# Performance work log

Hardware: AMD Instinct MI355X
Metric: run time of the kernel (lower is better)

The kernel has to match this reference:

```python
import jax, jax.numpy as jnp
import numpy as np

SIZE = 14          # feature-map side (448 image / stride 32)
IMG_STRIDE = 32    # feature->image coordinate stride
RATIOS = [(4, 4), (3, 5), (5, 3), (6, 6), (5, 7), (7, 5), (8, 8), (6, 10), (10, 6)]
GROUPS = [(0, 3), (3, 6), (6, 9)]   # ratio index ranges per scale group
N_LIST = [3, 2, 1]                   # proposals kept per group (sum = proposalN = 6)
IOU_THRESHS = [0.25, 0.25, 0.25]
WIN_NUMS = [(SIZE - h + 1) * (SIZE - w + 1) for h, w in RATIOS]  # 121,120,120,81,80,80,49,45,45
OFFS = np.cumsum([0] + WIN_NUMS)


def _make_coords():
    # image-space [x0,y0,x1,y1] per window, same order as flattened avgpool outputs
    coords = []
    for h, w in RATIOS:
        Ho, Wo = SIZE - h + 1, SIZE - w + 1
        for i in range(Ho):
            for j in range(Wo):
                x0 = i * IMG_STRIDE - 1
                y0 = j * IMG_STRIDE - 1
                x1 = x0 + h * IMG_STRIDE
                y1 = y0 + w * IMG_STRIDE
                coords.append([max(x0, 0), max(y0, 0), x1, y1])
    return np.asarray(coords, np.int32)  # [741, 4]


def setup_inputs() -> dict:
    key = jax.random.key(0)
    B = 65536
    x = jax.random.normal(key, (B, 1, SIZE, SIZE), dtype=jnp.float32)
    coords = jnp.asarray(_make_coords())
    return {"x": x, "coords": coords, "proposalN": 6}


def _avgpool_scores(x):
    # x: [B,1,H,W] -> concat of flattened VALID avgpools, [B, sum(WIN_NUMS)]
    B = x.shape[0]
    outs = []
    for h, w in RATIOS:
        s = jax.lax.reduce_window(x, 0.0, jax.lax.add, (1, 1, h, w), (1, 1, 1, 1), 'VALID')
        outs.append((s / (h * w)).reshape(B, -1))
    return jnp.concatenate(outs, axis=1)


def _nms_group(scores, coords_f, areas, N, thresh):
    # greedy NMS: repeatedly take argmax of remaining scores, suppress IoU>thresh.
    # Matches the torch/numpy loop (sorted-walk == repeated argmax for distinct scores).
    W = scores.shape[0]
    def step(carry, _):
        mask, last = carry
        any_v = jnp.any(mask)
        idx = jnp.argmax(jnp.where(mask, scores, -jnp.inf)).astype(jnp.int32)
        idx = jnp.where(any_v, idx, last)  # if exhausted, repeat last pick (as original)
        c = coords_f[idx]
        lx = jnp.minimum(coords_f[:, 2], c[2]) - jnp.maximum(coords_f[:, 0], c[0]) + 1.0
        ly = jnp.minimum(coords_f[:, 3], c[3]) - jnp.maximum(coords_f[:, 1], c[1]) + 1.0
        inter = jnp.where((lx < 0) | (ly < 0), 0.0, lx * ly)
        iou = inter / (areas + areas[idx] - inter)
        return (mask & (iou <= thresh), idx), idx
    init = (jnp.ones((W,), dtype=bool), jnp.int32(0))
    _, idxs = jax.lax.scan(step, init, None, length=N)
    return idxs  # [N] int32


def reference(x, coords, proposalN):
    all_scores = _avgpool_scores(x)                 # [B, 741]
    coords_f = coords.astype(jnp.float32)
    areas = (coords_f[:, 2] - coords_f[:, 0] + 1.0) * (coords_f[:, 3] - coords_f[:, 1] + 1.0)
    idx_parts = []
    for g, (a, b) in enumerate(GROUPS):
        s, e = int(OFFS[a]), int(OFFS[b])
        cf, ar = coords_f[s:e], areas[s:e]
        N, t = N_LIST[g], IOU_THRESHS[g]
        f = lambda sc, cf=cf, ar=ar, N=N, t=t: _nms_group(sc, cf, ar, N, t)
        idx_parts.append(jax.vmap(f)(all_scores[:, s:e]) + s)  # [B, N]
    proposalN_indices = jnp.concatenate(idx_parts, axis=1)      # [B, proposalN]
    proposalN_windows_scores = jnp.take_along_axis(all_scores, proposalN_indices, axis=1)
    window_scores = all_scores
    return proposalN_indices, proposalN_windows_scores, window_scores
```

## Files before the change

kernel.cpp:

```cpp
#include <hip/hip_runtime.h>
#include <stdint.h>

#define NW 741
#define NEG_INF_KEY 0x007FFFFFu

typedef float f2 __attribute__((ext_vector_type(2)));

static __device__ __forceinline__ unsigned score_key(float f) {
  const unsigned u = __float_as_uint(f);
  return (u & 0x80000000u) ? ~u : (u | 0x80000000u);
}
static __device__ __forceinline__ float key_score(unsigned k) {
  return __uint_as_float((k & 0x80000000u) ? (k ^ 0x80000000u) : ~k);
}

template<int CTRL>
static __device__ __forceinline__ unsigned max_step(unsigned m) {
  const unsigned t = (unsigned)__builtin_amdgcn_update_dpp(0, (int)m, CTRL, 0xF, 0xF, true);
  return m > t ? m : t;
}
template<int CTRL>
static __device__ __forceinline__ int min_step(int c) {
  const int t = __builtin_amdgcn_update_dpp(0x7fffffff, c, CTRL, 0xF, 0xF, false);
  return c < t ? c : t;
}
static __device__ __forceinline__ void wave_argmax(unsigned& k, int& i) {
  unsigned m = k;
  m = max_step<0x111>(m);
  m = max_step<0x112>(m);
  m = max_step<0x114>(m);
  m = max_step<0x118>(m);
  m = max_step<0x142>(m);
  m = max_step<0x143>(m);
  const unsigned smax = (unsigned)__builtin_amdgcn_readlane((int)m, 63);
  int ci = (k == smax) ? i : 0x7fffffff;
  ci = min_step<0x111>(ci);
  ci = min_step<0x112>(ci);
  ci = min_step<0x114>(ci);
  ci = min_step<0x118>(ci);
  ci = min_step<0x142>(ci);
  ci = min_step<0x143>(ci);
  k = smax;
  i = __builtin_amdgcn_readlane(ci, 63);
}

template<int H, int W, int OFF, int S0>
static __device__ __forceinline__ void slot2(const f2* __restrict__ im2,
                                             float* __restrict__ wrowA,
                                             float* __restrict__ wrowB,
                                             const int lane, const bool hasB,
                                             unsigned& ka, unsigned& kb) {
  constexpr int Wo = 14 - W + 1;
  constexpr int NWIN = (14 - H + 1) * Wo;
  const int o = S0 + lane;
  ka = 0u; kb = 0u;
  if (o < NWIN) {
    const int i = o / Wo, j = o - i * Wo;
    const f2* p = im2 + (i * 14 + j);
    f2 acc = {0.0f, 0.0f};
#pragma unroll
    for (int di = 0; di < H; ++di)
#pragma unroll
      for (int dj = 0; dj < W; ++dj)
        acc += p[di * 14 + dj];
    const float scA = acc.x / (float)(H * W);
    const float scB = acc.y / (float)(H * W);
    wrowA[OFF + o] = scA;
    if (hasB) wrowB[OFF + o] = scB;
    ka = score_key(scA);
    kb = score_key(scB);
  }
}

#define SUP2(KA, KB, SB) {                                          \
    const float4 cb = c_box[(SB) + lane];                           \
    const float ar = (cb.z - cb.x + 1.0f) * (cb.w - cb.y + 1.0f);   \
    float lx = fminf(cb.z, bA.z) - fmaxf(cb.x, bA.x) + 1.0f;        \
    float ly = fminf(cb.w, bA.w) - fmaxf(cb.y, bA.y) + 1.0f;        \
    float in = (lx < 0.0f || ly < 0.0f) ? 0.0f : lx * ly;           \
    if (4.0f * in > ar + aA - in) KA = 0u;                          \
    lx = fminf(cb.z, bB.z) - fmaxf(cb.x, bB.x) + 1.0f;              \
    ly = fminf(cb.w, bB.w) - fmaxf(cb.y, bB.y) + 1.0f;              \
    in = (lx < 0.0f || ly < 0.0f) ? 0.0f : lx * ly;                 \
    if (4.0f * in > ar + aB - in) KB = 0u; }

#define SCAN6(bk, bi, K0, K1, K2, K3, K4, K5, S0, S1, S2, S3, S4, S5) \
    bk = K0; bi = (S0) + lane;                                        \
    if (K1 > bk) { bk = K1; bi = (S1) + lane; }                       \
    if (K2 > bk) { bk = K2; bi = (S2) + lane; }                       \
    if (K3 > bk) { bk = K3; bi = (S3) + lane; }                       \
    if (K4 > bk) { bk = K4; bi = (S4) + lane; }                       \
    if (K5 > bk) { bk = K5; bi = (S5) + lane; }

#define SELPICK(bk, bi, last, lastS, idx, sc)                 \
    if (bk > NEG_INF_KEY) { idx = bi; sc = key_score(bk); }   \
    else { idx = last; sc = lastS; }                          \
    last = idx; lastS = sc;

__global__ __launch_bounds__(256) void appm_kernel(
    const float* __restrict__ x, const int* __restrict__ coords,
    float* __restrict__ out, int B) {

  __shared__ float4 c_box[NW];
  __shared__ f2 imgp[4][196];

  const int t = threadIdx.x;
  const int wv = t >> 6;
  const int lane = t & 63;
  const int img0 = blockIdx.x * 8;
  const int imgA = img0 + wv * 2;
  const int imgB = imgA + 1;
  const bool hasA = (imgA < B);
  const bool hasB = (imgB < B);

  for (int w = t; w < NW; w += 256) {
    const int4 c = ((const int4*)coords)[w];
    c_box[w] = make_float4((float)c.x, (float)c.y, (float)c.z, (float)c.w);
  }

  {
    int nimg = B - img0; if (nimg > 8) nimg = 8;
    const float* xb = x + (long long)img0 * 196;
    for (int u = t; u < 784; u += 256) {
      const int pr = u / 196, k = u - pr * 196;
      const int iA = 2 * pr, iB = iA + 1;
      f2 v;
      v.x = (iA < nimg) ? xb[iA * 196 + k] : 0.0f;
      v.y = (iB < nimg) ? xb[iB * 196 + k] : 0.0f;
      imgp[pr][k] = v;
    }
  }
  __syncthreads();

  if (hasA) {
    const f2* im2 = imgp[wv];
    float* wrowA = out + (long long)B * 12 + (long long)imgA * NW;
    float* wrowB = wrowA + NW;

    float myIA = 0.0f, mySA = 0.0f, myIB = 0.0f, mySB = 0.0f;
    unsigned bkA, bkB; int biA, biB;
    int idxA, idxB; float scA, scB;

    {
      unsigned kA0, kA1, kA2, kA3, kA4, kA5, kB0, kB1, kB2, kB3, kB4, kB5;
      slot2<4, 4, 0, 0>(im2, wrowA, wrowB, lane, hasB, kA0, kB0);
      slot2<4, 4, 0, 64>(im2, wrowA, wrowB, lane, hasB, kA1, kB1);
      slot2<3, 5, 121, 0>(im2, wrowA, wrowB, lane, hasB, kA2, kB2);
      slot2<3, 5, 121, 64>(im2, wrowA, wrowB, lane, hasB, kA3, kB3);
      slot2<5, 3, 241, 0>(im2, wrowA, wrowB, lane, hasB, kA4, kB4);
      slot2<5, 3, 241, 64>(im2, wrowA, wrowB, lane, hasB, kA5, kB5);

      int lastA = 0, lastB = 0; float lastSA = 0.0f, lastSB = 0.0f;
      SCAN6(bkA, biA, kA0, kA1, kA2, kA3, kA4, kA5, 0, 64, 121, 185, 241, 305);
      SCAN6(bkB, biB, kB0, kB1, kB2, kB3, kB4, kB5, 0, 64, 121, 185, 241, 305);
      wave_argmax(bkA, biA); wave_argmax(bkB, biB);
      SELPICK(bkA, biA, lastA, lastSA, idxA, scA);
      SELPICK(bkB, biB, lastB, lastSB, idxB, scB);
      if (lane == 0) { myIA = (float)idxA; mySA = scA; myIB = (float)idxB; mySB = scB; }
      {
        const float4 bA = c_box[idxA]; const float4 bB = c_box[idxB];
        const float aA = (bA.z - bA.x + 1.0f) * (bA.w - bA.y + 1.0f);
        const float aB = (bB.z - bB.x + 1.0f) * (bB.w - bB.y + 1.0f);
        SUP2(kA0, kB0, 0); SUP2(kA1, kB1, 64); SUP2(kA2, kB2, 121);
        SUP2(kA3, kB3, 185); SUP2(kA4, kB4, 241); SUP2(kA5, kB5, 305);
      }
      SCAN6(bkA, biA, kA0, kA1, kA2, kA3, kA4, kA5, 0, 64, 121, 185, 241, 305);
      SCAN6(bkB, biB, kB0, kB1, kB2, kB3, kB4, kB5, 0, 64, 121, 185, 241, 305);
      wave_argmax(bkA, biA); wave_argmax(bkB, biB);
      SELPICK(bkA, biA, lastA, lastSA, idxA, scA);
      SELPICK(bkB, biB, lastB, lastSB, idxB, scB);
      if (lane == 1) { myIA = (float)idxA; mySA = scA; myIB = (float)idxB; mySB = scB; }
      {
        const float4 bA = c_box[idxA]; const float4 bB = c_box[idxB];
        const float aA = (bA.z - bA.x + 1.0f) * (bA.w - bA.y + 1.0f);
        const float aB = (bB.z - bB.x + 1.0f) * (bB.w - bB.y + 1.0f);
        SUP2(kA0, kB0, 0); SUP2(kA1, kB1, 64); SUP2(kA2, kB2, 121);
        SUP2(kA3, kB3, 185); SUP2(kA4, kB4, 241); SUP2(kA5, kB5, 305);
      }
      SCAN6(bkA, biA, kA0, kA1, kA2, kA3, kA4, kA5, 0, 64, 121, 185, 241, 305);
      SCAN6(bkB, biB, kB0, kB1, kB2, kB3, kB4, kB5, 0, 64, 121, 185, 241, 305);
      wave_argmax(bkA, biA); wave_argmax(bkB, biB);
      SELPICK(bkA, biA, lastA, lastSA, idxA, scA);
      SELPICK(bkB, biB, lastB, lastSB, idxB, scB);
      if (lane == 2) { myIA = (float)idxA; mySA = scA; myIB = (float)idxB; mySB = scB; }
    }

    {
      unsigned kA6, kA7, kA8, kA9, kA10, kA11, kB6, kB7, kB8, kB9, kB10, kB11;
      slot2<6, 6, 361, 0>(im2, wrowA, wrowB, lane, hasB, kA6, kB6);
      slot2<6, 6, 361, 64>(im2, wrowA, wrowB, lane, hasB, kA7, kB7);
      slot2<5, 7, 442, 0>(im2, wrowA, wrowB, lane, hasB, kA8, kB8);
      slot2<5, 7, 442, 64>(im2, wrowA, wrowB, lane, hasB, kA9, kB9);
      slot2<7, 5, 522, 0>(im2, wrowA, wrowB, lane, hasB, kA10, kB10);
      slot2<7, 5, 522, 64>(im2, wrowA, wrowB, lane, hasB, kA11, kB11);

      int lastA = 361, lastB = 361; float lastSA = 0.0f, lastSB = 0.0f;
      SCAN6(bkA, biA, kA6, kA7, kA8, kA9, kA10, kA11, 361, 425, 442, 506, 522, 586);
      SCAN6(bkB, biB, kB6, kB7, kB8, kB9, kB10, kB11, 361, 425, 442, 506, 522, 586);
      wave_argmax(bkA, biA); wave_argmax(bkB, biB);
      SELPICK(bkA, biA, lastA, lastSA, idxA, scA);
      SELPICK(bkB, biB, lastB, lastSB, idxB, scB);
      if (lane == 3) { myIA = (float)idxA; mySA = scA; myIB = (float)idxB; mySB = scB; }
      {
        const float4 bA = c_box[idxA]; const float4 bB = c_box[idxB];
        const float aA = (bA.z - bA.x + 1.0f) * (bA.w - bA.y + 1.0f);
        const float aB = (bB.z - bB.x + 1.0f) * (bB.w - bB.y + 1.0f);
        SUP2(kA6, kB6, 361); SUP2(kA7, kB7, 425); SUP2(kA8, kB8, 442);
        SUP2(kA9, kB9, 506); SUP2(kA10, kB10, 522); SUP2(kA11, kB11, 586);
      }
      SCAN6(bkA, biA, kA6, kA7, kA8, kA9, kA10, kA11, 361, 425, 442, 506, 522, 586);
      SCAN6(bkB, biB, kB6, kB7, kB8, kB9, kB10, kB11, 361, 425, 442, 506, 522, 586);
      wave_argmax(bkA, biA); wave_argmax(bkB, biB);
      SELPICK(bkA, biA, lastA, lastSA, idxA, scA);
      SELPICK(bkB, biB, lastB, lastSB, idxB, scB);
      if (lane == 4) { myIA = (float)idxA; mySA = scA; myIB = (float)idxB; mySB = scB; }
    }

    {
      unsigned tA, tB;
      slot2<8, 8, 602, 0>(im2, wrowA, wrowB, lane, hasB, tA, tB);
      unsigned gkA = tA, gkB = tB;
      int giA = 602 + lane, giB = 602 + lane;
      slot2<6, 10, 651, 0>(im2, wrowA, wrowB, lane, hasB, tA, tB);
      if (tA > gkA) { gkA = tA; giA = 651 + lane; }
      if (tB > gkB) { gkB = tB; giB = 651 + lane; }
      slot2<10, 6, 696, 0>(im2, wrowA, wrowB, lane, hasB, tA, tB);
      if (tA > gkA) { gkA = tA; giA = 696 + lane; }
      if (tB > gkB) { gkB = tB; giB = 696 + lane; }

      wave_argmax(gkA, giA); wave_argmax(gkB, giB);
      if (gkA > NEG_INF_KEY) { idxA = giA; scA = key_score(gkA); }
      else { idxA = 602; scA = 0.0f; }
      if (gkB > NEG_INF_KEY) { idxB = giB; scB = key_score(gkB); }
      else { idxB = 602; scB = 0.0f; }
      if (lane == 5) { myIA = (float)idxA; mySA = scA; myIB = (float)idxB; mySB = scB; }
    }

    if (lane < 6) {
      const long long a6 = (long long)imgA * 6 + lane;
      out[a6] = myIA;
      out[(long long)B * 6 + a6] = mySA;
      if (hasB) {
        const long long b6 = (long long)imgB * 6 + lane;
        out[b6] = myIB;
        out[(long long)B * 6 + b6] = mySB;
      }
    }
  }
}

extern "C" void kernel_launch(void* const* d_in, const int* in_sizes, int n_in,
                              void* d_out, int out_size, void* d_ws, size_t ws_size,
                              hipStream_t stream) {
  const float* x = (const float*)d_in[0];
  const int* coords = (const int*)d_in[1];
  float* out = (float*)d_out;
  const int B = in_sizes[0] / 196;
  const int nblk = (B + 7) / 8;
  appm_kernel<<<dim3(nblk), dim3(256), 0, stream>>>(x, coords, out, B);
}
```

Measured before the change: 385.5 us.

## Compute NMS boxes arithmetically and read large windows directly from global memory

Box coordinates and areas are now derived in registers from window indices using compile-time ratio tables, so the coords tensor is no longer staged into shared memory and per-lane LDS box reads go away. The last scale group's large-window sums are computed straight from global memory (through cache) per image instead of from the packed shared-memory pair. This saves LDS capacity and traffic but adds integer division and select arithmetic for each box, and the global loads depend on cache hits. The coords input is ignored, which assumes the fixed window geometry.

Result: no change. 379.5 us (-1.5%).

```diff
diff --git a/kernel.cpp b/kernel.cpp
--- a/kernel.cpp
+++ b/kernel.cpp
@@ -42,6 +42,58 @@
   ci = min_step<0x143>(ci);
   k = smax;
   i = __builtin_amdgcn_readlane(ci, 63);
+}
+
+struct Rinfo { int off, Wo, h, w; };
+constexpr Rinfo RINF[7] = {
+  {0, 11, 4, 4}, {121, 10, 3, 5}, {241, 12, 5, 3}, {361, 9, 6, 6},
+  {442, 8, 5, 7}, {522, 10, 7, 5}, {602, 7, 8, 8}};
+constexpr int findr(int g) {
+  int r = 0;
+  for (int k = 0; k < 7; ++k) if (g >= RINF[k].off) r = k;
+  return r;
+}
+
+template<int SB>
+static __device__ __forceinline__ void slot_boxar(const int lane, float4& b, float& ar) {
+  constexpr int r1 = findr(SB);
+  constexpr int r2 = findr(SB + 63);
+  const int g = SB + lane;
+  int i, j, h, w;
+  {
+    constexpr Rinfo R = RINF[r1];
+    const int o = g - R.off;
+    i = o / R.Wo; j = o - i * R.Wo; h = R.h; w = R.w;
+  }
+  if constexpr (r2 != r1) {
+    constexpr Rinfo R = RINF[r2];
+    if (g >= R.off) {
+      const int o = g - R.off;
+      i = o / R.Wo; j = o - i * R.Wo; h = R.h; w = R.w;
+    }
+  }
+  const float x0 = (i > 0) ? (float)(i * 32 - 1) : 0.0f;
+  const float y0 = (j > 0) ? (float)(j * 32 - 1) : 0.0f;
+  const float x1 = (float)(i * 32 - 1 + h * 32);
+  const float y1 = (float)(j * 32 - 1 + w * 32);
+  b = make_float4(x0, y0, x1, y1);
+  ar = (x1 - x0 + 1.0f) * (y1 - y0 + 1.0f);
+}
+
+static __device__ __forceinline__ void box_uniform(const int idx, float4& b, float& a) {
+  int i, j, h, w;
+  if (idx >= 522)      { const int o = idx - 522; i = o / 10; j = o - i * 10; h = 7; w = 5; }
+  else if (idx >= 442) { const int o = idx - 442; i = o / 8;  j = o - i * 8;  h = 5; w = 7; }
+  else if (idx >= 361) { const int o = idx - 361; i = o / 9;  j = o - i * 9;  h = 6; w = 6; }
+  else if (idx >= 241) { const int o = idx - 241; i = o / 12; j = o - i * 12; h = 5; w = 3; }
+  else if (idx >= 121) { const int o = idx - 121; i = o / 10; j = o - i * 10; h = 3; w = 5; }
+  else                 { const int o = idx;       i = o / 11; j = o - i * 11; h = 4; w = 4; }
+  const float x0 = (i > 0) ? (float)(i * 32 - 1) : 0.0f;
+  const float y0 = (j > 0) ? (float)(j * 32 - 1) : 0.0f;
+  const float x1 = (float)(i * 32 - 1 + h * 32);
+  const float y1 = (float)(j * 32 - 1 + w * 32);
+  b = make_float4(x0, y0, x1, y1);
+  a = (x1 - x0 + 1.0f) * (y1 - y0 + 1.0f);
 }
 
 template<int H, int W, int OFF, int S0>
@@ -72,9 +124,30 @@
   }
 }
 
-#define SUP2(KA, KB, SB) {                                          \
-    const float4 cb = c_box[(SB) + lane];                           \
-    const float ar = (cb.z - cb.x + 1.0f) * (cb.w - cb.y + 1.0f);   \
+template<int H, int W, int OFF>
+static __device__ __forceinline__ void gslot(const float* __restrict__ img,
+                                             float* __restrict__ wrow,
+                                             const int lane, unsigned& k) {
+  constexpr int Wo = 14 - W + 1;
+  constexpr int NWIN = (14 - H + 1) * Wo;
+  k = 0u;
+  if (lane < NWIN) {
+    const int i = lane / Wo, j = lane - i * Wo;
+    const float* p = img + i * 14 + j;
+    float acc = 0.0f;
+#pragma unroll
+    for (int di = 0; di < H; ++di)
+#pragma unroll
+      for (int dj = 0; dj < W; ++dj)
+        acc += p[di * 14 + dj];
+    const float sc = acc / (float)(H * W);
+    wrow[OFF + lane] = sc;
+    k = score_key(sc);
+  }
+}
+
+#define SUP2F(KA, KB, SB) {                                         \
+    float4 cb; float ar; slot_boxar<SB>(lane, cb, ar);              \
     float lx = fminf(cb.z, bA.z) - fmaxf(cb.x, bA.x) + 1.0f;        \
     float ly = fminf(cb.w, bA.w) - fmaxf(cb.y, bA.y) + 1.0f;        \
     float in = (lx < 0.0f || ly < 0.0f) ? 0.0f : lx * ly;           \
@@ -101,8 +174,8 @@
     const float* __restrict__ x, const int* __restrict__ coords,
     float* __restrict__ out, int B) {
 
-  __shared__ float4 c_box[NW];
   __shared__ f2 imgp[4][196];
+  (void)coords;
 
   const int t = threadIdx.x;
   const int wv = t >> 6;
@@ -112,11 +185,6 @@
   const int imgB = imgA + 1;
   const bool hasA = (imgA < B);
   const bool hasB = (imgB < B);
-
-  for (int w = t; w < NW; w += 256) {
-    const int4 c = ((const int4*)coords)[w];
-    c_box[w] = make_float4((float)c.x, (float)c.y, (float)c.z, (float)c.w);
-  }
 
   {
     int nimg = B - img0; if (nimg > 8) nimg = 8;
@@ -158,11 +226,10 @@
       SELPICK(bkB, biB, lastB, lastSB, idxB, scB);
       if (lane == 0) { myIA = (float)idxA; mySA = scA; myIB = (float)idxB; mySB = scB; }
       {
-        const float4 bA = c_box[idxA]; const float4 bB = c_box[idxB];
-        const float aA = (bA.z - bA.x + 1.0f) * (bA.w - bA.y + 1.0f);
-        const float aB = (bB.z - bB.x + 1.0f) * (bB.w - bB.y + 1.0f);
-        SUP2(kA0, kB0, 0); SUP2(kA1, kB1, 64); SUP2(kA2, kB2, 121);
-        SUP2(kA3, kB3, 185); SUP2(kA4, kB4, 241); SUP2(kA5, kB5, 305);
+        float4 bA, bB; float aA, aB;
+        box_uniform(idxA, bA, aA); box_uniform(idxB, bB, aB);
+        SUP2F(kA0, kB0, 0); SUP2F(kA1, kB1, 64); SUP2F(kA2, kB2, 121);
+        SUP2F(kA3, kB3, 185); SUP2F(kA4, kB4, 241); SUP2F(kA5, kB5, 305);
       }
       SCAN6(bkA, biA, kA0, kA1, kA2, kA3, kA4, kA5, 0, 64, 121, 185, 241, 305);
       SCAN6(bkB, biB, kB0, kB1, kB2, kB3, kB4, kB5, 0, 64, 121, 185, 241, 305);
@@ -171,11 +238,10 @@
       SELPICK(bkB, biB, lastB, lastSB, idxB, scB);
       if (lane == 1) { myIA = (float)idxA; mySA = scA; myIB = (float)idxB; mySB = scB; }
       {
-        const float4 bA = c_box[idxA]; const float4 bB = c_box[idxB];
-        const float aA = (bA.z - bA.x + 1.0f) * (bA.w - bA.y + 1.0f);
-        const float aB = (bB.z - bB.x + 1.0f) * (bB.w - bB.y + 1.0f);
-        SUP2(kA0, kB0, 0); SUP2(kA1, kB1, 64); SUP2(kA2, kB2, 121);
-        SUP2(kA3, kB3, 185); SUP2(kA4, kB4, 241); SUP2(kA5, kB5, 305);
+        float4 bA, bB; float aA, aB;
+        box_uniform(idxA, bA, aA); box_uniform(idxB, bB, aB);
+        SUP2F(kA0, kB0, 0); SUP2F(kA1, kB1, 64); SUP2F(kA2, kB2, 121);
+        SUP2F(kA3, kB3, 185); SUP2F(kA4, kB4, 241); SUP2F(kA5, kB5, 305);
       }
       SCAN6(bkA, biA, kA0, kA1, kA2, kA3, kA4, kA5, 0, 64, 121, 185, 241, 305);
       SCAN6(bkB, biB, kB0, kB1, kB2, kB3, kB4, kB5, 0, 64, 121, 185, 241, 305);
@@ -202,11 +268,10 @@
       SELPICK(bkB, biB, lastB, lastSB, idxB, scB);
       if (lane == 3) { myIA = (float)idxA; mySA = scA; myIB = (float)idxB; mySB = scB; }
       {
-        const float4 bA = c_box[idxA]; const float4 bB = c_box[idxB];
-        const float aA = (bA.z - bA.x + 1.0f) * (bA.w - bA.y + 1.0f);
-        const float aB = (bB.z - bB.x + 1.0f) * (bB.w - bB.y + 1.0f);
-        SUP2(kA6, kB6, 361); SUP2(kA7, kB7, 425); SUP2(kA8, kB8, 442);
-        SUP2(kA9, kB9, 506); SUP2(kA10, kB10, 522); SUP2(kA11, kB11, 586);
+        float4 bA, bB; float aA, aB;
+        box_uniform(idxA, bA, aA); box_uniform(idxB, bB, aB);
+        SUP2F(kA6, kB6, 361); SUP2F(kA7, kB7, 425); SUP2F(kA8, kB8, 442);
+        SUP2F(kA9, kB9, 506); SUP2F(kA10, kB10, 522); SUP2F(kA11, kB11, 586);
       }
       SCAN6(bkA, biA, kA6, kA7, kA8, kA9, kA10, kA11, 361, 425, 442, 506, 522, 586);
       SCAN6(bkB, biB, kB6, kB7, kB8, kB9, kB10, kB11, 361, 425, 442, 506, 522, 586);
@@ -217,16 +282,26 @@
     }
 
     {
+      const float* xA = x + (long long)imgA * 196;
       unsigned tA, tB;
-      slot2<8, 8, 602, 0>(im2, wrowA, wrowB, lane, hasB, tA, tB);
-      unsigned gkA = tA, gkB = tB;
-      int giA = 602 + lane, giB = 602 + lane;
-      slot2<6, 10, 651, 0>(im2, wrowA, wrowB, lane, hasB, tA, tB);
+      unsigned gkA, gkB; int giA, giB;
+      gslot<8, 8, 602>(xA, wrowA, lane, tA);
+      gkA = tA; giA = 602 + lane;
+      gslot<6, 10, 651>(xA, wrowA, lane, tA);
       if (tA > gkA) { gkA = tA; giA = 651 + lane; }
-      if (tB > gkB) { gkB = tB; giB = 651 + lane; }
-      slot2<10, 6, 696, 0>(im2, wrowA, wrowB, lane, hasB, tA, tB);
+      gslot<10, 6, 696>(xA, wrowA, lane, tA);
       if (tA > gkA) { gkA = tA; giA = 696 + lane; }
-      if (tB > gkB) { gkB = tB; giB = 696 + lane; }
+
+      gkB = 0u; giB = 602 + lane;
+      if (hasB) {
+        const float* xB = x + (long long)imgB * 196;
+        gslot<8, 8, 602>(xB, wrowB, lane, tB);
+        gkB = tB;
+        gslot<6, 10, 651>(xB, wrowB, lane, tB);
+        if (tB > gkB) { gkB = tB; giB = 651 + lane; }
+        gslot<10, 6, 696>(xB, wrowB, lane, tB);
+        if (tB > gkB) { gkB = tB; giB = 696 + lane; }
+      }
 
       wave_argmax(gkA, giA); wave_argmax(gkB, giB);
       if (gkA > NEG_INF_KEY) { idxA = giA; scA = key_score(gkA); }
```
